# Performance work log

Hardware: AMD Instinct MI355X
Metric: run time of the kernel (lower is better)

The kernel has to match this reference:

```python
import jax, jax.numpy as jnp
import numpy as np

# config[4]: SparseConv3d(32, 64, k=3, stride=2, pad=1) on a (21,800,704) voxel grid, nnz=220939
IN_DIMS = (21, 800, 704)   # (x, y, z) spatial extents
KSIZE   = (3, 3, 3)
STRIDE  = (2, 2, 2)
PAD     = (1, 1, 1)
CIN, COUT = 32, 64
NNZ = 220939
OUT_DIMS = tuple((IN_DIMS[d] + 2 * PAD[d] - KSIZE[d]) // STRIDE[d] + 1 for d in range(3))  # (11,400,352)


def setup_inputs() -> dict:
    key = jax.random.key(0)
    k1, k2, k3 = jax.random.split(key, 3)
    features = jax.random.normal(k1, (NNZ, CIN), dtype=jnp.float32)
    coords = jnp.stack(
        [jax.random.randint(jax.random.fold_in(k2, d), (NNZ,), 0, IN_DIMS[d]) for d in range(3)],
        axis=1,
    ).astype(jnp.int32)
    # spconv weight layout: one [Cin, Cout] GEMM per kernel offset (27 offsets)
    weight = jax.random.normal(k3, (KSIZE[0] * KSIZE[1] * KSIZE[2], CIN, COUT), dtype=jnp.float32) * 0.05
    return {"features": features, "coords": coords, "weight": weight}


def reference(features, coords, weight):
    # Rulebook gather-GEMM-scatter, vectorized over points; static loop over 27 offsets.
    # out[o] += W[k] @ in[i] where i = o*stride - pad + k, i.e. o = (coord_i + pad - k)/stride.
    n_out = OUT_DIMS[0] * OUT_DIMS[1] * OUT_DIMS[2]
    stride = jnp.array(STRIDE, jnp.int32)
    pad = jnp.array(PAD, jnp.int32)
    odims = jnp.array(OUT_DIMS, jnp.int32)
    out = jnp.zeros((n_out + 1, COUT), features.dtype)  # last row = dump slot for invalid
    kidx = 0
    for kx in range(KSIZE[0]):
        for ky in range(KSIZE[1]):
            for kz in range(KSIZE[2]):
                off = jnp.array([kx, ky, kz], jnp.int32)
                o = coords + pad - off                      # [N,3]
                oq = o // stride
                valid = jnp.all((o >= 0) & (o % stride == 0) & (oq < odims), axis=1)
                flat = (oq[:, 0] * OUT_DIMS[1] + oq[:, 1]) * OUT_DIMS[2] + oq[:, 2]
                flat = jnp.where(valid, flat, n_out)
                contrib = features @ weight[kidx]           # [N, Cout] per-offset GEMM
                out = out.at[flat].add(contrib)             # scatter-accumulate
                kidx += 1
    # Densified sparse-conv output (inactive output sites are exactly zero)
    return out[:-1].reshape(OUT_DIMS + (COUT,))
```

## Files before the change

kernel.cpp:

```cpp
#include <hip/hip_runtime.h>


#define CIN    32
#define COUT   64
#define OXD    11
#define OYD    400
#define OZD    352
#define NOUT   (OXD * OYD * OZD)
#define BSITES 128
#define NBUCK  (NOUT / BSITES)
#define CAP    256
#define OVCAP  32768
#define NWT    (27 * COUT * CIN)

typedef float v2f __attribute__((ext_vector_type(2)));

__global__ __launch_bounds__(256) void prep(const float* __restrict__ w,
                                            float* __restrict__ wt,
                                            int* __restrict__ gcnt,
                                            int* __restrict__ ovcnt) {
    const int i = blockIdx.x * 256 + threadIdx.x;
    if (i < NWT) {
        const int k  = i >> 11;
        const int rm = i & 2047;
        const int co = rm >> 5;
        const int ci = rm & 31;
        wt[i] = w[k * (CIN * COUT) + ci * COUT + co];
    }
    if (i < NBUCK) gcnt[i] = 0;
    if (i == NBUCK) *ovcnt = 0;
}

__global__ __launch_bounds__(256) void build_pairs(
    const int* __restrict__ coords,
    int* __restrict__ arena,
    int* __restrict__ gcnt,
    int* __restrict__ ovcnt,
    int2* __restrict__ ovlist,
    int nnz)
{
    const int n = blockIdx.x * 256 + threadIdx.x;
    if (n >= nnz) return;

    const int cx = coords[3 * n + 0];
    const int cy = coords[3 * n + 1];
    const int cz = coords[3 * n + 2];

    int kxl[2], oxl[2], nx;
    int kyl[2], oyl[2], ny;
    int kzl[2], ozl[2], nz;
    {
        const int c1 = cx + 1;
        if (c1 & 1) { kxl[0] = 1; oxl[0] = c1 >> 1; nx = 1; }
        else { kxl[0] = 2; oxl[0] = (c1 - 2) >> 1; nx = 1;
               if ((c1 >> 1) < OXD) { kxl[1] = 0; oxl[1] = c1 >> 1; nx = 2; } }
    }
    {
        const int c1 = cy + 1;
        if (c1 & 1) { kyl[0] = 1; oyl[0] = c1 >> 1; ny = 1; }
        else { kyl[0] = 2; oyl[0] = (c1 - 2) >> 1; ny = 1;
               if ((c1 >> 1) < OYD) { kyl[1] = 0; oyl[1] = c1 >> 1; ny = 2; } }
    }
    {
        const int c1 = cz + 1;
        if (c1 & 1) { kzl[0] = 1; ozl[0] = c1 >> 1; nz = 1; }
        else { kzl[0] = 2; ozl[0] = (c1 - 2) >> 1; nz = 1;
               if ((c1 >> 1) < OZD) { kzl[1] = 0; ozl[1] = c1 >> 1; nz = 2; } }
    }

    for (int ix = 0; ix < nx; ++ix)
        for (int iy = 0; iy < ny; ++iy)
            for (int iz = 0; iz < nz; ++iz) {
                const int k    = kxl[ix] * 9 + kyl[iy] * 3 + kzl[iz];
                const int site = (oxl[ix] * OYD + oyl[iy]) * OZD + ozl[iz];
                const int bkt  = site >> 7;
                const int loc  = site & (BSITES - 1);
                const int slot = atomicAdd(&gcnt[bkt], 1);
                if (slot < CAP) {
                    arena[(size_t)bkt * CAP + slot] = (n << 12) | (k << 7) | loc;
                } else {
                    const int o = atomicAdd(ovcnt, 1);
                    if (o < OVCAP) ovlist[o] = make_int2(site, (n << 5) | k);
                }
            }
}

__global__ __launch_bounds__(256, 4) void spconv_scatter(
    const float* __restrict__ feat,
    const float* __restrict__ wt,
    const int*   __restrict__ arena,
    const int*   __restrict__ gcnt,
    float*       __restrict__ out)
{
    __shared__ float tile[BSITES][COUT];
    __shared__ int   sorted[CAP];
    __shared__ int   khist[27];
    __shared__ int   kbase[27];

    const int t    = threadIdx.x;
    const int lane = t & 63;
    const int wid  = t >> 6;
    const int b    = blockIdx.x;
    const int cnt  = min(gcnt[b], CAP);

    if (t < 27) khist[t] = 0;
    __syncthreads();

    int myp = 0, myk = 0;
    if (t < cnt) {
        myp = arena[(size_t)b * CAP + t];
        myk = (myp >> 7) & 31;
        atomicAdd(&khist[myk], 1);
    }
    float4* t4 = (float4*)&tile[0][0];
    #pragma unroll
    for (int r = 0; r < 8; ++r) t4[t + r * 256] = make_float4(0.f, 0.f, 0.f, 0.f);
    __syncthreads();

    if (wid == 0) {
        const int h = (lane < 27) ? khist[lane] : 0;
        int v = h;
        #pragma unroll
        for (int off = 1; off < 32; off <<= 1) {
            const int u = __shfl_up(v, off);
            if (lane >= off) v += u;
        }
        if (lane < 27) kbase[lane] = v - h;
    }
    __syncthreads();
    if (t < cnt) {
        const int pos = atomicAdd(&kbase[myk], 1);
        sorted[pos] = myp;
    }
    __syncthreads();

    const int c  = (cnt + 3) >> 2;
    const int jb = min(wid * c, cnt);
    const int je = min(jb + c, cnt);
    float4 wv[8];
    int curk = -1;
    for (int j = jb; j < je; ++j) {
        const int pk  = __builtin_amdgcn_readfirstlane(sorted[j]);
        const int k   = (pk >> 7) & 31;
        const int loc = pk & (BSITES - 1);
        const int pt  = pk >> 12;
        if (k != curk) {
            curk = k;
            const float4* __restrict__ wp =
                (const float4*)(wt + ((size_t)k * COUT + lane) * CIN);
            #pragma unroll
            for (int bb = 0; bb < 8; ++bb) wv[bb] = wp[bb];
        }
        const float4* __restrict__ fp = (const float4*)(feat + (size_t)pt * CIN);
        v2f a0 = {0.f, 0.f}, a1 = {0.f, 0.f};
        #pragma unroll
        for (int bb = 0; bb < 8; ++bb) {
            const float4 f = fp[bb];
            const float4 wb = wv[bb];
            v2f f01 = {f.x, f.y}, f23 = {f.z, f.w};
            v2f w01 = {wb.x, wb.y}, w23 = {wb.z, wb.w};
#if __has_builtin(__builtin_elementwise_fma)
            a0 = __builtin_elementwise_fma(f01, w01, a0);
            a1 = __builtin_elementwise_fma(f23, w23, a1);
#else
            a0[0] = fmaf(f01[0], w01[0], a0[0]);
            a0[1] = fmaf(f01[1], w01[1], a0[1]);
            a1[0] = fmaf(f23[0], w23[0], a1[0]);
            a1[1] = fmaf(f23[1], w23[1], a1[1]);
#endif
        }
        atomicAdd(&tile[loc][lane], (a0[0] + a0[1]) + (a1[0] + a1[1]));
    }
    __syncthreads();

    float4* __restrict__ o4 = (float4*)(out + (size_t)b * (BSITES * COUT));
    #pragma unroll
    for (int r = 0; r < 8; ++r) o4[t + r * 256] = t4[t + r * 256];
}

__global__ __launch_bounds__(256) void fixup_overflow(
    const float* __restrict__ feat,
    const float* __restrict__ wt,
    const int2*  __restrict__ ovlist,
    const int*   __restrict__ ovcnt,
    float*       __restrict__ out)
{
    const int lane = threadIdx.x & 63;
    const int gw   = blockIdx.x * 4 + (threadIdx.x >> 6);
    const int n    = min(*ovcnt, OVCAP);
    for (int e = gw; e < n; e += 128 * 4) {
        const int2 r   = ovlist[e];
        const int site = r.x;
        const int pt   = r.y >> 5;
        const int k    = r.y & 31;
        const float4* __restrict__ wp =
            (const float4*)(wt + ((size_t)k * COUT + lane) * CIN);
        const float4* __restrict__ fp = (const float4*)(feat + (size_t)pt * CIN);
        float acc = 0.f;
        #pragma unroll
        for (int bb = 0; bb < 8; ++bb) {
            const float4 f = fp[bb];
            const float4 w = wp[bb];
            acc = fmaf(f.x, w.x, acc);
            acc = fmaf(f.y, w.y, acc);
            acc = fmaf(f.z, w.z, acc);
            acc = fmaf(f.w, w.w, acc);
        }
        atomicAdd(out + (size_t)site * COUT + lane, acc);
    }
}

extern "C" void kernel_launch(void* const* d_in, const int* in_sizes, int n_in,
                              void* d_out, int out_size, void* d_ws, size_t ws_size,
                              hipStream_t stream) {
    const float* feat   = (const float*)d_in[0];
    const int*   coords = (const int*)d_in[1];
    const float* weight = (const float*)d_in[2];
    float*       out    = (float*)d_out;
    const int nnz = in_sizes[0] / CIN;

    float* WT     = (float*)d_ws;
    int*   gcnt   = (int*)(WT + NWT);
    int*   ovcnt  = gcnt + NBUCK;
    int2*  ovlist = (int2*)(ovcnt + 2);
    int*   arena  = (int*)(ovlist + OVCAP);

    prep<<<(NWT + 255) / 256, 256, 0, stream>>>(weight, WT, gcnt, ovcnt);
    build_pairs<<<(nnz + 255) / 256, 256, 0, stream>>>(coords, arena, gcnt,
                                                       ovcnt, ovlist, nnz);
    spconv_scatter<<<NBUCK, 256, 0, stream>>>(feat, WT, arena, gcnt, out);
    fixup_overflow<<<128, 256, 0, stream>>>(feat, WT, ovlist, ovcnt, out);
}
```

Before: 675.8 us.

## Stage feature rows cooperatively in LDS and pad bucket counters

Each wave now loads the pair list into registers once. It then fetches feature rows 16 at a time with coalesced per-lane float4 loads into a swizzled LDS staging buffer. Before, every lane re-read the same row from global memory for each pair in sequence. This exposes more memory-level parallelism and cuts redundant broadcast loads. Bucket counters are spread 16 ints apart so atomics on neighbouring buckets do not share a cache line, and spconv_scatter's launch-bounds occupancy hint drops from 4 to 3 blocks to leave room for the extra LDS and registers.

Result: slower. 715.8 us (+5.9%).

```diff
diff --git a/kernel.cpp b/kernel.cpp
--- a/kernel.cpp
+++ b/kernel.cpp
@@ -10,6 +10,7 @@
 #define BSITES 128
 #define NBUCK  (NOUT / BSITES)
 #define CAP    256
+#define GSTR   16
 #define OVCAP  32768
 #define NWT    (27 * COUT * CIN)
 
@@ -27,8 +28,8 @@
         const int ci = rm & 31;
         wt[i] = w[k * (CIN * COUT) + ci * COUT + co];
     }
-    if (i < NBUCK) gcnt[i] = 0;
-    if (i == NBUCK) *ovcnt = 0;
+    if (i < NBUCK) gcnt[i * GSTR] = 0;
+    if (i == 0) *ovcnt = 0;
 }
 
 __global__ __launch_bounds__(256) void build_pairs(
@@ -75,7 +76,7 @@
                 const int site = (oxl[ix] * OYD + oyl[iy]) * OZD + ozl[iz];
                 const int bkt  = site >> 7;
                 const int loc  = site & (BSITES - 1);
-                const int slot = atomicAdd(&gcnt[bkt], 1);
+                const int slot = atomicAdd(&gcnt[bkt * GSTR], 1);
                 if (slot < CAP) {
                     arena[(size_t)bkt * CAP + slot] = (n << 12) | (k << 7) | loc;
                 } else {
@@ -85,7 +86,7 @@
             }
 }
 
-__global__ __launch_bounds__(256, 4) void spconv_scatter(
+__global__ __launch_bounds__(256, 3) void spconv_scatter(
     const float* __restrict__ feat,
     const float* __restrict__ wt,
     const int*   __restrict__ arena,
@@ -93,6 +94,7 @@
     float*       __restrict__ out)
 {
     __shared__ float tile[BSITES][COUT];
+    __shared__ float fstage[4][16 * 32];
     __shared__ int   sorted[CAP];
     __shared__ int   khist[27];
     __shared__ int   kbase[27];
@@ -101,7 +103,7 @@
     const int lane = t & 63;
     const int wid  = t >> 6;
     const int b    = blockIdx.x;
-    const int cnt  = min(gcnt[b], CAP);
+    const int cnt  = min(gcnt[b * GSTR], CAP);
 
     if (t < 27) khist[t] = 0;
     __syncthreads();
@@ -137,39 +139,60 @@
     const int c  = (cnt + 3) >> 2;
     const int jb = min(wid * c, cnt);
     const int je = min(jb + c, cnt);
+
+    const int vp = sorted[(jb + lane < je) ? (jb + lane) : (je > jb ? je - 1 : 0)];
+
+    float* __restrict__ fs = &fstage[wid][0];
     float4 wv[8];
     int curk = -1;
-    for (int j = jb; j < je; ++j) {
-        const int pk  = __builtin_amdgcn_readfirstlane(sorted[j]);
-        const int k   = (pk >> 7) & 31;
-        const int loc = pk & (BSITES - 1);
-        const int pt  = pk >> 12;
-        if (k != curk) {
-            curk = k;
-            const float4* __restrict__ wp =
-                (const float4*)(wt + ((size_t)k * COUT + lane) * CIN);
+
+    for (int g0 = jb; g0 < je; g0 += 16) {
+        #pragma unroll
+        for (int i = 0; i < 2; ++i) {
+            const int r   = (lane >> 3) + 8 * i;
+            const int s   = min(g0 - jb + r, je - 1 - jb);
+            const int pv  = __shfl(vp, s);
+            const int pt  = pv >> 12;
+            const int ch  = lane & 7;
+            const float4 v = ((const float4*)(feat + (size_t)pt * CIN))[ch];
+            const int sw  = ch ^ (r & 7);
+            *(float4*)(fs + (r * 8 + sw) * 4) = v;
+        }
+        asm volatile("s_waitcnt lgkmcnt(0)" ::: "memory");
+
+        const int jend = min(g0 + 16, je);
+        for (int j = g0; j < jend; ++j) {
+            const int pk  = __builtin_amdgcn_readlane(vp, j - jb);
+            const int k   = (pk >> 7) & 31;
+            const int loc = pk & (BSITES - 1);
+            const int r   = j - g0;
+            if (k != curk) {
+                curk = k;
+                const float4* __restrict__ wp =
+                    (const float4*)(wt + ((size_t)k * COUT + lane) * CIN);
+                #pragma unroll
+                for (int bb = 0; bb < 8; ++bb) wv[bb] = wp[bb];
+            }
+            v2f a0 = {0.f, 0.f}, a1 = {0.f, 0.f};
             #pragma unroll
-            for (int bb = 0; bb < 8; ++bb) wv[bb] = wp[bb];
-        }
-        const float4* __restrict__ fp = (const float4*)(feat + (size_t)pt * CIN);
-        v2f a0 = {0.f, 0.f}, a1 = {0.f, 0.f};
-        #pragma unroll
-        for (int bb = 0; bb < 8; ++bb) {
-            const float4 f = fp[bb];
-            const float4 wb = wv[bb];
-            v2f f01 = {f.x, f.y}, f23 = {f.z, f.w};
-            v2f w01 = {wb.x, wb.y}, w23 = {wb.z, wb.w};
+            for (int bb = 0; bb < 8; ++bb) {
+                const float4 f =
+                    *(const float4*)(fs + (r * 8 + (bb ^ (r & 7))) * 4);
+                const float4 wb = wv[bb];
+                v2f f01 = {f.x, f.y}, f23 = {f.z, f.w};
+                v2f w01 = {wb.x, wb.y}, w23 = {wb.z, wb.w};
 #if __has_builtin(__builtin_elementwise_fma)
-            a0 = __builtin_elementwise_fma(f01, w01, a0);
-            a1 = __builtin_elementwise_fma(f23, w23, a1);
+                a0 = __builtin_elementwise_fma(f01, w01, a0);
+                a1 = __builtin_elementwise_fma(f23, w23, a1);
 #else
-            a0[0] = fmaf(f01[0], w01[0], a0[0]);
-            a0[1] = fmaf(f01[1], w01[1], a0[1]);
-            a1[0] = fmaf(f23[0], w23[0], a1[0]);
-            a1[1] = fmaf(f23[1], w23[1], a1[1]);
+                a0[0] = fmaf(f01[0], w01[0], a0[0]);
+                a0[1] = fmaf(f01[1], w01[1], a0[1]);
+                a1[0] = fmaf(f23[0], w23[0], a1[0]);
+                a1[1] = fmaf(f23[1], w23[1], a1[1]);
 #endif
-        }
-        atomicAdd(&tile[loc][lane], (a0[0] + a0[1]) + (a1[0] + a1[1]));
+            }
+            atomicAdd(&tile[loc][lane], (a0[0] + a0[1]) + (a1[0] + a1[1]));
+        }
     }
     __syncthreads();
 
@@ -221,7 +244,7 @@
 
     float* WT     = (float*)d_ws;
     int*   gcnt   = (int*)(WT + NWT);
-    int*   ovcnt  = gcnt + NBUCK;
+    int*   ovcnt  = gcnt + NBUCK * GSTR;
     int2*  ovlist = (int2*)(ovcnt + 2);
     int*   arena  = (int*)(ovlist + OVCAP);
 
```

## Replace bucketed scatter rulebook with dense voxel map and per-output gather

Applied to the files above, without the earlier changes.

Swaps the atomic-bucketed pair arena for a dense input-voxel index map filled by atomicExch. Each output block then probes the 27 neighbours of its sites through the map and accumulates contributions in a shared-memory tile. Duplicate coordinates go to a dup list that a fixup kernel scatters with global atomics. This removes the global bucket atomics and the in-block sort, but adds clearing a ~47MB map and many mostly-empty random probes.

Measured after the change: 929.8 us. +37.6%, slower.

```diff
diff --git a/kernel.cpp b/kernel.cpp
--- a/kernel.cpp
+++ b/kernel.cpp
@@ -3,23 +3,28 @@
 
 #define CIN    32
 #define COUT   64
+#define IXD    21
+#define IYD    800
+#define IZD    704
 #define OXD    11
 #define OYD    400
 #define OZD    352
 #define NOUT   (OXD * OYD * OZD)
+#define NVOX   (IXD * IYD * IZD)
+#define NVOX4  (NVOX / 4)
 #define BSITES 128
-#define NBUCK  (NOUT / BSITES)
-#define CAP    256
-#define OVCAP  32768
+#define NBLK   (NOUT / BSITES)
 #define NWT    (27 * COUT * CIN)
+#define DUPCAP 48000
 
 typedef float v2f __attribute__((ext_vector_type(2)));
 
 __global__ __launch_bounds__(256) void prep(const float* __restrict__ w,
+                                            int4* __restrict__ map4,
                                             float* __restrict__ wt,
-                                            int* __restrict__ gcnt,
-                                            int* __restrict__ ovcnt) {
+                                            int* __restrict__ dupcnt) {
     const int i = blockIdx.x * 256 + threadIdx.x;
+    if (i < NVOX4) map4[i] = make_int4(-1, -1, -1, -1);
     if (i < NWT) {
         const int k  = i >> 11;
         const int rm = i & 2047;
@@ -27,186 +32,182 @@
         const int ci = rm & 31;
         wt[i] = w[k * (CIN * COUT) + ci * COUT + co];
     }
-    if (i < NBUCK) gcnt[i] = 0;
-    if (i == NBUCK) *ovcnt = 0;
-}
-
-__global__ __launch_bounds__(256) void build_pairs(
+    if (i == 0) *dupcnt = 0;
+}
+
+__global__ __launch_bounds__(256) void build_map(
     const int* __restrict__ coords,
-    int* __restrict__ arena,
-    int* __restrict__ gcnt,
-    int* __restrict__ ovcnt,
-    int2* __restrict__ ovlist,
+    int* __restrict__ map,
+    int* __restrict__ dupcnt,
+    int* __restrict__ duplist,
     int nnz)
 {
     const int n = blockIdx.x * 256 + threadIdx.x;
     if (n >= nnz) return;
-
     const int cx = coords[3 * n + 0];
     const int cy = coords[3 * n + 1];
     const int cz = coords[3 * n + 2];
-
-    int kxl[2], oxl[2], nx;
-    int kyl[2], oyl[2], ny;
-    int kzl[2], ozl[2], nz;
-    {
-        const int c1 = cx + 1;
-        if (c1 & 1) { kxl[0] = 1; oxl[0] = c1 >> 1; nx = 1; }
-        else { kxl[0] = 2; oxl[0] = (c1 - 2) >> 1; nx = 1;
-               if ((c1 >> 1) < OXD) { kxl[1] = 0; oxl[1] = c1 >> 1; nx = 2; } }
-    }
-    {
-        const int c1 = cy + 1;
-        if (c1 & 1) { kyl[0] = 1; oyl[0] = c1 >> 1; ny = 1; }
-        else { kyl[0] = 2; oyl[0] = (c1 - 2) >> 1; ny = 1;
-               if ((c1 >> 1) < OYD) { kyl[1] = 0; oyl[1] = c1 >> 1; ny = 2; } }
-    }
-    {
-        const int c1 = cz + 1;
-        if (c1 & 1) { kzl[0] = 1; ozl[0] = c1 >> 1; nz = 1; }
-        else { kzl[0] = 2; ozl[0] = (c1 - 2) >> 1; nz = 1;
-               if ((c1 >> 1) < OZD) { kzl[1] = 0; ozl[1] = c1 >> 1; nz = 2; } }
-    }
-
-    for (int ix = 0; ix < nx; ++ix)
-        for (int iy = 0; iy < ny; ++iy)
-            for (int iz = 0; iz < nz; ++iz) {
-                const int k    = kxl[ix] * 9 + kyl[iy] * 3 + kzl[iz];
-                const int site = (oxl[ix] * OYD + oyl[iy]) * OZD + ozl[iz];
-                const int bkt  = site >> 7;
-                const int loc  = site & (BSITES - 1);
-                const int slot = atomicAdd(&gcnt[bkt], 1);
-                if (slot < CAP) {
-                    arena[(size_t)bkt * CAP + slot] = (n << 12) | (k << 7) | loc;
-                } else {
-                    const int o = atomicAdd(ovcnt, 1);
-                    if (o < OVCAP) ovlist[o] = make_int2(site, (n << 5) | k);
-                }
-            }
-}
-
-__global__ __launch_bounds__(256, 4) void spconv_scatter(
+    const int v  = (cx * IYD + cy) * IZD + cz;
+    const int old = atomicExch(&map[v], n);
+    if (old >= 0) {
+        const int s = atomicAdd(dupcnt, 1);
+        if (s < DUPCAP) duplist[s] = old;
+    }
+}
+
+__global__ __launch_bounds__(256, 4) void spconv_gather(
     const float* __restrict__ feat,
     const float* __restrict__ wt,
-    const int*   __restrict__ arena,
-    const int*   __restrict__ gcnt,
+    const int*   __restrict__ map,
     float*       __restrict__ out)
 {
     __shared__ float tile[BSITES][COUT];
-    __shared__ int   sorted[CAP];
-    __shared__ int   khist[27];
-    __shared__ int   kbase[27];
 
     const int t    = threadIdx.x;
     const int lane = t & 63;
     const int wid  = t >> 6;
-    const int b    = blockIdx.x;
-    const int cnt  = min(gcnt[b], CAP);
-
-    if (t < 27) khist[t] = 0;
-    __syncthreads();
-
-    int myp = 0, myk = 0;
-    if (t < cnt) {
-        myp = arena[(size_t)b * CAP + t];
-        myk = (myp >> 7) & 31;
-        atomicAdd(&khist[myk], 1);
-    }
+
     float4* t4 = (float4*)&tile[0][0];
     #pragma unroll
     for (int r = 0; r < 8; ++r) t4[t + r * 256] = make_float4(0.f, 0.f, 0.f, 0.f);
     __syncthreads();
 
-    if (wid == 0) {
-        const int h = (lane < 27) ? khist[lane] : 0;
-        int v = h;
+    const int ls   = lane & 31;
+    const int site = blockIdx.x * BSITES + wid * 32 + ls;
+    const int ox   = site / (OYD * OZD);
+    const int r0   = site - ox * (OYD * OZD);
+    const int oy   = r0 / OZD;
+    const int oz   = r0 - oy * OZD;
+    const int ix0  = 2 * ox - 1;
+    const int iy0  = 2 * oy - 1;
+    const int iz0  = 2 * oz - 1;
+    const int kh   = lane >> 5;
+
+    auto probe = [&](int kp) -> int {
+        const int kk = kp + kh;
+        if (kk >= 27) return -1;
+        const int kx = kk / 9;
+        const int kr = kk - kx * 9;
+        const int ky = kr / 3;
+        const int kz = kr - ky * 3;
+        const int ix = ix0 + kx, iy = iy0 + ky, iz = iz0 + kz;
+        if ((unsigned)ix >= IXD || (unsigned)iy >= IYD || (unsigned)iz >= IZD)
+            return -1;
+        return map[(ix * IYD + iy) * IZD + iz];
+    };
+
+    int v = probe(0);
+    for (int kp = 0; kp < 27; kp += 2) {
+        const int vnext = (kp + 2 < 27) ? probe(kp + 2) : -1;
+        const unsigned long long bal = __ballot(v >= 0);
         #pragma unroll
-        for (int off = 1; off < 32; off <<= 1) {
-            const int u = __shfl_up(v, off);
-            if (lane >= off) v += u;
-        }
-        if (lane < 27) kbase[lane] = v - h;
-    }
-    __syncthreads();
-    if (t < cnt) {
-        const int pos = atomicAdd(&kbase[myk], 1);
-        sorted[pos] = myp;
-    }
-    __syncthreads();
-
-    const int c  = (cnt + 3) >> 2;
-    const int jb = min(wid * c, cnt);
-    const int je = min(jb + c, cnt);
-    float4 wv[8];
-    int curk = -1;
-    for (int j = jb; j < je; ++j) {
-        const int pk  = __builtin_amdgcn_readfirstlane(sorted[j]);
-        const int k   = (pk >> 7) & 31;
-        const int loc = pk & (BSITES - 1);
-        const int pt  = pk >> 12;
-        if (k != curk) {
-            curk = k;
+        for (int s = 0; s < 2; ++s) {
+            const int k = kp + s;
+            if (k >= 27) break;
+            unsigned mask = (unsigned)(bal >> (32 * s));
+            if (mask == 0) continue;
+            float4 wv[8];
             const float4* __restrict__ wp =
                 (const float4*)(wt + ((size_t)k * COUT + lane) * CIN);
             #pragma unroll
-            for (int bb = 0; bb < 8; ++bb) wv[bb] = wp[bb];
-        }
-        const float4* __restrict__ fp = (const float4*)(feat + (size_t)pt * CIN);
-        v2f a0 = {0.f, 0.f}, a1 = {0.f, 0.f};
-        #pragma unroll
-        for (int bb = 0; bb < 8; ++bb) {
-            const float4 f = fp[bb];
-            const float4 wb = wv[bb];
-            v2f f01 = {f.x, f.y}, f23 = {f.z, f.w};
-            v2f w01 = {wb.x, wb.y}, w23 = {wb.z, wb.w};
+            for (int b = 0; b < 8; ++b) wv[b] = wp[b];
+            do {
+                const int bit = __builtin_ctz(mask);
+                mask &= mask - 1;
+                const int p = __builtin_amdgcn_readlane(v, 32 * s + bit);
+                const float4* __restrict__ fr4 =
+                    (const float4*)(feat + (size_t)p * CIN);
+                float4 fr[8];
+                #pragma unroll
+                for (int b = 0; b < 8; ++b) fr[b] = fr4[b];
+                v2f a0 = {0.f, 0.f}, a1 = {0.f, 0.f};
+                #pragma unroll
+                for (int b = 0; b < 8; ++b) {
+                    v2f f01 = {fr[b].x, fr[b].y}, f23 = {fr[b].z, fr[b].w};
+                    v2f w01 = {wv[b].x, wv[b].y}, w23 = {wv[b].z, wv[b].w};
 #if __has_builtin(__builtin_elementwise_fma)
-            a0 = __builtin_elementwise_fma(f01, w01, a0);
-            a1 = __builtin_elementwise_fma(f23, w23, a1);
+                    a0 = __builtin_elementwise_fma(f01, w01, a0);
+                    a1 = __builtin_elementwise_fma(f23, w23, a1);
 #else
-            a0[0] = fmaf(f01[0], w01[0], a0[0]);
-            a0[1] = fmaf(f01[1], w01[1], a0[1]);
-            a1[0] = fmaf(f23[0], w23[0], a1[0]);
-            a1[1] = fmaf(f23[1], w23[1], a1[1]);
+                    a0[0] = fmaf(f01[0], w01[0], a0[0]);
+                    a0[1] = fmaf(f01[1], w01[1], a0[1]);
+                    a1[0] = fmaf(f23[0], w23[0], a1[0]);
+                    a1[1] = fmaf(f23[1], w23[1], a1[1]);
 #endif
-        }
-        atomicAdd(&tile[loc][lane], (a0[0] + a0[1]) + (a1[0] + a1[1]));
+                }
+                atomicAdd(&tile[wid * 32 + bit][lane],
+                          (a0[0] + a0[1]) + (a1[0] + a1[1]));
+            } while (mask);
+        }
+        v = vnext;
     }
     __syncthreads();
 
-    float4* __restrict__ o4 = (float4*)(out + (size_t)b * (BSITES * COUT));
+    float4* __restrict__ o4 = (float4*)(out + (size_t)blockIdx.x * (BSITES * COUT));
     #pragma unroll
     for (int r = 0; r < 8; ++r) o4[t + r * 256] = t4[t + r * 256];
 }
 
-__global__ __launch_bounds__(256) void fixup_overflow(
+__global__ __launch_bounds__(256) void fixup_dups(
     const float* __restrict__ feat,
     const float* __restrict__ wt,
-    const int2*  __restrict__ ovlist,
-    const int*   __restrict__ ovcnt,
+    const int*   __restrict__ coords,
+    const int*   __restrict__ duplist,
+    const int*   __restrict__ dupcnt,
     float*       __restrict__ out)
 {
     const int lane = threadIdx.x & 63;
     const int gw   = blockIdx.x * 4 + (threadIdx.x >> 6);
-    const int n    = min(*ovcnt, OVCAP);
-    for (int e = gw; e < n; e += 128 * 4) {
-        const int2 r   = ovlist[e];
-        const int site = r.x;
-        const int pt   = r.y >> 5;
-        const int k    = r.y & 31;
-        const float4* __restrict__ wp =
-            (const float4*)(wt + ((size_t)k * COUT + lane) * CIN);
-        const float4* __restrict__ fp = (const float4*)(feat + (size_t)pt * CIN);
-        float acc = 0.f;
+    const int n    = min(*dupcnt, DUPCAP);
+    for (int e = gw; e < n; e += 64 * 4) {
+        const int p  = duplist[e];
+        const int cx = coords[3 * p + 0];
+        const int cy = coords[3 * p + 1];
+        const int cz = coords[3 * p + 2];
+        int kxl[2], oxl[2], nx;
+        int kyl[2], oyl[2], ny;
+        int kzl[2], ozl[2], nz;
+        {
+            const int c1 = cx + 1;
+            if (c1 & 1) { kxl[0] = 1; oxl[0] = c1 >> 1; nx = 1; }
+            else { kxl[0] = 2; oxl[0] = (c1 - 2) >> 1; nx = 1;
+                   if ((c1 >> 1) < OXD) { kxl[1] = 0; oxl[1] = c1 >> 1; nx = 2; } }
+        }
+        {
+            const int c1 = cy + 1;
+            if (c1 & 1) { kyl[0] = 1; oyl[0] = c1 >> 1; ny = 1; }
+            else { kyl[0] = 2; oyl[0] = (c1 - 2) >> 1; ny = 1;
+                   if ((c1 >> 1) < OYD) { kyl[1] = 0; oyl[1] = c1 >> 1; ny = 2; } }
+        }
+        {
+            const int c1 = cz + 1;
+            if (c1 & 1) { kzl[0] = 1; ozl[0] = c1 >> 1; nz = 1; }
+            else { kzl[0] = 2; ozl[0] = (c1 - 2) >> 1; nz = 1;
+                   if ((c1 >> 1) < OZD) { kzl[1] = 0; ozl[1] = c1 >> 1; nz = 2; } }
+        }
+        const float4* __restrict__ fp = (const float4*)(feat + (size_t)p * CIN);
+        float4 fr[8];
         #pragma unroll
-        for (int bb = 0; bb < 8; ++bb) {
-            const float4 f = fp[bb];
-            const float4 w = wp[bb];
-            acc = fmaf(f.x, w.x, acc);
-            acc = fmaf(f.y, w.y, acc);
-            acc = fmaf(f.z, w.z, acc);
-            acc = fmaf(f.w, w.w, acc);
-        }
-        atomicAdd(out + (size_t)site * COUT + lane, acc);
+        for (int b = 0; b < 8; ++b) fr[b] = fp[b];
+        for (int ix = 0; ix < nx; ++ix)
+            for (int iy = 0; iy < ny; ++iy)
+                for (int iz = 0; iz < nz; ++iz) {
+                    const int k    = kxl[ix] * 9 + kyl[iy] * 3 + kzl[iz];
+                    const int site = (oxl[ix] * OYD + oyl[iy]) * OZD + ozl[iz];
+                    const float4* __restrict__ wp =
+                        (const float4*)(wt + ((size_t)k * COUT + lane) * CIN);
+                    float acc = 0.f;
+                    #pragma unroll
+                    for (int b = 0; b < 8; ++b) {
+                        const float4 f = fr[b];
+                        const float4 w = wp[b];
+                        acc = fmaf(f.x, w.x, acc);
+                        acc = fmaf(f.y, w.y, acc);
+                        acc = fmaf(f.z, w.z, acc);
+                        acc = fmaf(f.w, w.w, acc);
+                    }
+                    atomicAdd(out + (size_t)site * COUT + lane, acc);
+                }
     }
 }
 
@@ -219,15 +220,14 @@
     float*       out    = (float*)d_out;
     const int nnz = in_sizes[0] / CIN;
 
-    float* WT     = (float*)d_ws;
-    int*   gcnt   = (int*)(WT + NWT);
-    int*   ovcnt  = gcnt + NBUCK;
-    int2*  ovlist = (int2*)(ovcnt + 2);
-    int*   arena  = (int*)(ovlist + OVCAP);
-
-    prep<<<(NWT + 255) / 256, 256, 0, stream>>>(weight, WT, gcnt, ovcnt);
-    build_pairs<<<(nnz + 255) / 256, 256, 0, stream>>>(coords, arena, gcnt,
-                                                       ovcnt, ovlist, nnz);
-    spconv_scatter<<<NBUCK, 256, 0, stream>>>(feat, WT, arena, gcnt, out);
-    fixup_overflow<<<128, 256, 0, stream>>>(feat, WT, ovlist, ovcnt, out);
-}
+    int*   map     = (int*)d_ws;
+    float* WT      = (float*)(map + NVOX);
+    int*   dupcnt  = (int*)(WT + NWT);
+    int*   duplist = dupcnt + 4;
+
+    prep<<<(NVOX4 + 255) / 256, 256, 0, stream>>>(weight, (int4*)map, WT, dupcnt);
+    build_map<<<(nnz + 255) / 256, 256, 0, stream>>>(coords, map, dupcnt,
+                                                     duplist, nnz);
+    spconv_gather<<<NBLK, 256, 0, stream>>>(feat, WT, map, out);
+    fixup_dups<<<64, 256, 0, stream>>>(feat, WT, coords, duplist, dupcnt, out);
+}
```

## Split sparse conv into per-offset GEMM and bucketed reduction with fp16 partials

Applied to the files above, without the earlier changes.

Pair building now emits two rulebooks: one grouped by kernel offset, filled through per-block shared-memory histograms and a single global atomic per offset, and one grouped by output bucket whose entries index into per-offset partial-product rows. A new per-offset kernel computes the 32x64 product for every pair and stores fp16 partials. The reduce kernel then only gathers those rows and accumulates them into a shared tile, so the per-bucket sorting and weight reloads go away. This adds a large intermediate buffer plus an extra pass, fp16 rounding of the partials, and a heavier overflow path when the per-offset capacity derived from workspace size is exceeded.

New measurement: 801.5 us. 18.6% more time.

```diff
diff --git a/kernel.cpp b/kernel.cpp
--- a/kernel.cpp
+++ b/kernel.cpp
@@ -10,14 +10,20 @@
 #define BSITES 128
 #define NBUCK  (NOUT / BSITES)
 #define CAP    256
-#define OVCAP  32768
+#define GSTR   16
 #define NWT    (27 * COUT * CIN)
+#define CHA    32
+#define PCAPK_MAX 32768
+#define OVCAP  600000
 
 typedef float v2f __attribute__((ext_vector_type(2)));
+typedef _Float16 half_t;
+typedef _Float16 h8 __attribute__((ext_vector_type(8)));
 
 __global__ __launch_bounds__(256) void prep(const float* __restrict__ w,
                                             float* __restrict__ wt,
-                                            int* __restrict__ gcnt,
+                                            int* __restrict__ kcnt,
+                                            int* __restrict__ bcnt,
                                             int* __restrict__ ovcnt) {
     const int i = blockIdx.x * 256 + threadIdx.x;
     if (i < NWT) {
@@ -27,149 +33,189 @@
         const int ci = rm & 31;
         wt[i] = w[k * (CIN * COUT) + ci * COUT + co];
     }
-    if (i < NBUCK) gcnt[i] = 0;
-    if (i == NBUCK) *ovcnt = 0;
-}
-
-__global__ __launch_bounds__(256) void build_pairs(
+    if (i < NBUCK) bcnt[i * GSTR] = 0;
+    if (i < 32)    kcnt[i] = 0;
+    if (i == 0)    *ovcnt = 0;
+}
+
+__global__ __launch_bounds__(512) void build_pairs(
     const int* __restrict__ coords,
-    int* __restrict__ arena,
-    int* __restrict__ gcnt,
+    int* __restrict__ arenaA,
+    int* __restrict__ arenaB,
+    int* __restrict__ kcnt,
+    int* __restrict__ bcnt,
     int* __restrict__ ovcnt,
     int2* __restrict__ ovlist,
-    int nnz)
-{
-    const int n = blockIdx.x * 256 + threadIdx.x;
-    if (n >= nnz) return;
-
-    const int cx = coords[3 * n + 0];
-    const int cy = coords[3 * n + 1];
-    const int cz = coords[3 * n + 2];
-
-    int kxl[2], oxl[2], nx;
-    int kyl[2], oyl[2], ny;
-    int kzl[2], ozl[2], nz;
-    {
-        const int c1 = cx + 1;
-        if (c1 & 1) { kxl[0] = 1; oxl[0] = c1 >> 1; nx = 1; }
-        else { kxl[0] = 2; oxl[0] = (c1 - 2) >> 1; nx = 1;
-               if ((c1 >> 1) < OXD) { kxl[1] = 0; oxl[1] = c1 >> 1; nx = 2; } }
-    }
-    {
-        const int c1 = cy + 1;
-        if (c1 & 1) { kyl[0] = 1; oyl[0] = c1 >> 1; ny = 1; }
-        else { kyl[0] = 2; oyl[0] = (c1 - 2) >> 1; ny = 1;
-               if ((c1 >> 1) < OYD) { kyl[1] = 0; oyl[1] = c1 >> 1; ny = 2; } }
-    }
-    {
-        const int c1 = cz + 1;
-        if (c1 & 1) { kzl[0] = 1; ozl[0] = c1 >> 1; nz = 1; }
-        else { kzl[0] = 2; ozl[0] = (c1 - 2) >> 1; nz = 1;
-               if ((c1 >> 1) < OZD) { kzl[1] = 0; ozl[1] = c1 >> 1; nz = 2; } }
-    }
-
-    for (int ix = 0; ix < nx; ++ix)
-        for (int iy = 0; iy < ny; ++iy)
-            for (int iz = 0; iz < nz; ++iz) {
-                const int k    = kxl[ix] * 9 + kyl[iy] * 3 + kzl[iz];
-                const int site = (oxl[ix] * OYD + oyl[iy]) * OZD + ozl[iz];
-                const int bkt  = site >> 7;
-                const int loc  = site & (BSITES - 1);
-                const int slot = atomicAdd(&gcnt[bkt], 1);
-                if (slot < CAP) {
-                    arena[(size_t)bkt * CAP + slot] = (n << 12) | (k << 7) | loc;
-                } else {
-                    const int o = atomicAdd(ovcnt, 1);
-                    if (o < OVCAP) ovlist[o] = make_int2(site, (n << 5) | k);
+    int nnz, int pcapk)
+{
+    __shared__ int lcnt[27];
+    __shared__ int lbase[27];
+    const int t = threadIdx.x;
+    if (t < 27) lcnt[t] = 0;
+    __syncthreads();
+
+    const int n = blockIdx.x * 512 + t;
+    int ncomb = 0;
+    int ck[8], cls[8], csite[8];
+    if (n < nnz) {
+        const int cx = coords[3 * n + 0];
+        const int cy = coords[3 * n + 1];
+        const int cz = coords[3 * n + 2];
+        int kxl[2], oxl[2], nx;
+        int kyl[2], oyl[2], ny;
+        int kzl[2], ozl[2], nz;
+        {
+            const int c1 = cx + 1;
+            if (c1 & 1) { kxl[0] = 1; oxl[0] = c1 >> 1; nx = 1; }
+            else { kxl[0] = 2; oxl[0] = (c1 - 2) >> 1; nx = 1;
+                   if ((c1 >> 1) < OXD) { kxl[1] = 0; oxl[1] = c1 >> 1; nx = 2; } }
+        }
+        {
+            const int c1 = cy + 1;
+            if (c1 & 1) { kyl[0] = 1; oyl[0] = c1 >> 1; ny = 1; }
+            else { kyl[0] = 2; oyl[0] = (c1 - 2) >> 1; ny = 1;
+                   if ((c1 >> 1) < OYD) { kyl[1] = 0; oyl[1] = c1 >> 1; ny = 2; } }
+        }
+        {
+            const int c1 = cz + 1;
+            if (c1 & 1) { kzl[0] = 1; ozl[0] = c1 >> 1; nz = 1; }
+            else { kzl[0] = 2; ozl[0] = (c1 - 2) >> 1; nz = 1;
+                   if ((c1 >> 1) < OZD) { kzl[1] = 0; ozl[1] = c1 >> 1; nz = 2; } }
+        }
+        for (int ix = 0; ix < nx; ++ix)
+            for (int iy = 0; iy < ny; ++iy)
+                for (int iz = 0; iz < nz; ++iz) {
+                    const int k = kxl[ix] * 9 + kyl[iy] * 3 + kzl[iz];
+                    ck[ncomb]    = k;
+                    csite[ncomb] = (oxl[ix] * OYD + oyl[iy]) * OZD + ozl[iz];
+                    cls[ncomb]   = atomicAdd(&lcnt[k], 1);
+                    ++ncomb;
                 }
+    }
+    __syncthreads();
+    if (t < 27) lbase[t] = atomicAdd(&kcnt[t], lcnt[t]);
+    __syncthreads();
+
+    for (int c = 0; c < ncomb; ++c) {
+        const int k     = ck[c];
+        const int site  = csite[c];
+        const int slotk = lbase[k] + cls[c];
+        if (slotk < pcapk) {
+            arenaA[(size_t)k * pcapk + slotk] = n;
+            const int bkt = site >> 7;
+            const int loc = site & (BSITES - 1);
+            const int sb  = atomicAdd(&bcnt[bkt * GSTR], 1);
+            if (sb < CAP) {
+                arenaB[(size_t)bkt * CAP + sb] = ((k * pcapk + slotk) << 7) | loc;
+            } else {
+                const int o = atomicAdd(ovcnt, 1);
+                if (o < OVCAP) ovlist[o] = make_int2(site, (n << 5) | k);
             }
-}
-
-__global__ __launch_bounds__(256, 4) void spconv_scatter(
+        } else {
+            const int o = atomicAdd(ovcnt, 1);
+            if (o < OVCAP) ovlist[o] = make_int2(site, (n << 5) | k);
+        }
+    }
+}
+
+__global__ __launch_bounds__(256, 3) void gemm_k(
     const float* __restrict__ feat,
     const float* __restrict__ wt,
-    const int*   __restrict__ arena,
-    const int*   __restrict__ gcnt,
-    float*       __restrict__ out)
+    const int*   __restrict__ arenaA,
+    const int*   __restrict__ kcnt,
+    half_t*      __restrict__ P16,
+    int pcapk)
+{
+    const int lane = threadIdx.x & 63;
+    const int wid  = threadIdx.x >> 6;
+    const int k     = blockIdx.x % 27;
+    const int chunk = blockIdx.x / 27;
+    const int cnt = min(kcnt[k], pcapk);
+    if (cnt == 0) return;
+
+    const int NW    = CHA * 4;
+    const int widk  = chunk * 4 + wid;
+    const int C     = (cnt + NW - 1) / NW;
+    const int start = min(widk * C, cnt);
+    const int end   = min(start + C, cnt);
+    const float* __restrict__ Wk = wt + (size_t)k * (COUT * CIN);
+    const int*   __restrict__ ak = arenaA + (size_t)k * pcapk;
+    half_t*      __restrict__ Pk = P16 + (size_t)k * pcapk * COUT;
+
+    for (int i0 = start; i0 < end; i0 += 64) {
+        const int idx = i0 + lane;
+        const int pt  = ak[min(idx, end - 1)];
+
+        v2f f[16];
+        {
+            const float4* __restrict__ fr4 = (const float4*)(feat + (size_t)pt * CIN);
+            #pragma unroll
+            for (int b = 0; b < 8; ++b) {
+                const float4 v = fr4[b];
+                f[2 * b + 0] = (v2f){v.x, v.y};
+                f[2 * b + 1] = (v2f){v.z, v.w};
+            }
+        }
+
+        if (idx < end) {
+            half_t* __restrict__ prow = Pk + (size_t)idx * COUT;
+            #pragma unroll
+            for (int g = 0; g < 8; ++g) {
+                h8 res;
+                #pragma unroll
+                for (int u = 0; u < 8; ++u) {
+                    const int co = 8 * g + u;
+                    const v2f* __restrict__ wv = (const v2f*)(Wk + co * CIN);
+                    v2f a = {0.f, 0.f};
+                    #pragma unroll
+                    for (int c2 = 0; c2 < 16; ++c2) {
+#if __has_builtin(__builtin_elementwise_fma)
+                        a = __builtin_elementwise_fma(f[c2], wv[c2], a);
+#else
+                        a[0] = fmaf(f[c2][0], wv[c2][0], a[0]);
+                        a[1] = fmaf(f[c2][1], wv[c2][1], a[1]);
+#endif
+                    }
+                    res[u] = (half_t)(a[0] + a[1]);
+                }
+                *(h8*)(prow + 8 * g) = res;
+            }
+        }
+    }
+}
+
+__global__ __launch_bounds__(256, 4) void reduce_b(
+    const half_t* __restrict__ P16,
+    const int*    __restrict__ arenaB,
+    const int*    __restrict__ bcnt,
+    float*        __restrict__ out)
 {
     __shared__ float tile[BSITES][COUT];
-    __shared__ int   sorted[CAP];
-    __shared__ int   khist[27];
-    __shared__ int   kbase[27];
 
     const int t    = threadIdx.x;
     const int lane = t & 63;
     const int wid  = t >> 6;
     const int b    = blockIdx.x;
-    const int cnt  = min(gcnt[b], CAP);
-
-    if (t < 27) khist[t] = 0;
-    __syncthreads();
-
-    int myp = 0, myk = 0;
-    if (t < cnt) {
-        myp = arena[(size_t)b * CAP + t];
-        myk = (myp >> 7) & 31;
-        atomicAdd(&khist[myk], 1);
-    }
+    const int cnt  = min(bcnt[b * GSTR], CAP);
+
     float4* t4 = (float4*)&tile[0][0];
     #pragma unroll
     for (int r = 0; r < 8; ++r) t4[t + r * 256] = make_float4(0.f, 0.f, 0.f, 0.f);
     __syncthreads();
 
-    if (wid == 0) {
-        const int h = (lane < 27) ? khist[lane] : 0;
-        int v = h;
-        #pragma unroll
-        for (int off = 1; off < 32; off <<= 1) {
-            const int u = __shfl_up(v, off);
-            if (lane >= off) v += u;
-        }
-        if (lane < 27) kbase[lane] = v - h;
-    }
-    __syncthreads();
-    if (t < cnt) {
-        const int pos = atomicAdd(&kbase[myk], 1);
-        sorted[pos] = myp;
-    }
-    __syncthreads();
-
     const int c  = (cnt + 3) >> 2;
     const int jb = min(wid * c, cnt);
     const int je = min(jb + c, cnt);
-    float4 wv[8];
-    int curk = -1;
+    const int* __restrict__ ab = arenaB + (size_t)b * CAP;
+    const int myw = ab[(jb + lane < je) ? (jb + lane) : (je > jb ? je - 1 : 0)];
+
+    #pragma unroll 8
     for (int j = jb; j < je; ++j) {
-        const int pk  = __builtin_amdgcn_readfirstlane(sorted[j]);
-        const int k   = (pk >> 7) & 31;
-        const int loc = pk & (BSITES - 1);
-        const int pt  = pk >> 12;
-        if (k != curk) {
-            curk = k;
-            const float4* __restrict__ wp =
-                (const float4*)(wt + ((size_t)k * COUT + lane) * CIN);
-            #pragma unroll
-            for (int bb = 0; bb < 8; ++bb) wv[bb] = wp[bb];
-        }
-        const float4* __restrict__ fp = (const float4*)(feat + (size_t)pt * CIN);
-        v2f a0 = {0.f, 0.f}, a1 = {0.f, 0.f};
-        #pragma unroll
-        for (int bb = 0; bb < 8; ++bb) {
-            const float4 f = fp[bb];
-            const float4 wb = wv[bb];
-            v2f f01 = {f.x, f.y}, f23 = {f.z, f.w};
-            v2f w01 = {wb.x, wb.y}, w23 = {wb.z, wb.w};
-#if __has_builtin(__builtin_elementwise_fma)
-            a0 = __builtin_elementwise_fma(f01, w01, a0);
-            a1 = __builtin_elementwise_fma(f23, w23, a1);
-#else
-            a0[0] = fmaf(f01[0], w01[0], a0[0]);
-            a0[1] = fmaf(f01[1], w01[1], a0[1]);
-            a1[0] = fmaf(f23[0], w23[0], a1[0]);
-            a1[1] = fmaf(f23[1], w23[1], a1[1]);
-#endif
-        }
-        atomicAdd(&tile[loc][lane], (a0[0] + a0[1]) + (a1[0] + a1[1]));
+        const int w    = __builtin_amdgcn_readlane(myw, j - jb);
+        const int prow = w >> 7;
+        const int loc  = w & (BSITES - 1);
+        const float h  = (float)P16[(size_t)prow * COUT + lane];
+        atomicAdd(&tile[loc][lane], h);
     }
     __syncthreads();
 
@@ -188,19 +234,19 @@
     const int lane = threadIdx.x & 63;
     const int gw   = blockIdx.x * 4 + (threadIdx.x >> 6);
     const int n    = min(*ovcnt, OVCAP);
-    for (int e = gw; e < n; e += 128 * 4) {
+    for (int e = gw; e < n; e += 64 * 4) {
         const int2 r   = ovlist[e];
         const int site = r.x;
-        const int pt   = r.y >> 5;
+        const int p    = r.y >> 5;
         const int k    = r.y & 31;
         const float4* __restrict__ wp =
             (const float4*)(wt + ((size_t)k * COUT + lane) * CIN);
-        const float4* __restrict__ fp = (const float4*)(feat + (size_t)pt * CIN);
+        const float4* __restrict__ fp = (const float4*)(feat + (size_t)p * CIN);
         float acc = 0.f;
         #pragma unroll
-        for (int bb = 0; bb < 8; ++bb) {
-            const float4 f = fp[bb];
-            const float4 w = wp[bb];
+        for (int b = 0; b < 8; ++b) {
+            const float4 f = fp[b];
+            const float4 w = wp[b];
             acc = fmaf(f.x, w.x, acc);
             acc = fmaf(f.y, w.y, acc);
             acc = fmaf(f.z, w.z, acc);
@@ -220,14 +266,27 @@
     const int nnz = in_sizes[0] / CIN;
 
     float* WT     = (float*)d_ws;
-    int*   gcnt   = (int*)(WT + NWT);
-    int*   ovcnt  = gcnt + NBUCK;
-    int2*  ovlist = (int2*)(ovcnt + 2);
-    int*   arena  = (int*)(ovlist + OVCAP);
-
-    prep<<<(NWT + 255) / 256, 256, 0, stream>>>(weight, WT, gcnt, ovcnt);
-    build_pairs<<<(nnz + 255) / 256, 256, 0, stream>>>(coords, arena, gcnt,
-                                                       ovcnt, ovlist, nnz);
-    spconv_scatter<<<NBUCK, 256, 0, stream>>>(feat, WT, arena, gcnt, out);
-    fixup_overflow<<<128, 256, 0, stream>>>(feat, WT, ovlist, ovcnt, out);
-}
+    int*   kcnt   = (int*)(WT + NWT);
+    int*   bcnt   = kcnt + 32;
+    int*   ovcnt  = bcnt + NBUCK * GSTR;
+    int*   arenaB = ovcnt + 4;
+    int2*  ovlist = (int2*)(arenaB + (size_t)NBUCK * CAP);
+    int*   arenaA = (int*)(ovlist + OVCAP);
+    const size_t fixed = (size_t)((char*)arenaA - (char*)d_ws);
+
+    long avail = (long)ws_size - (long)fixed - 512;
+    int pcapk = (int)(avail / (27L * (sizeof(int) + COUT * sizeof(half_t))));
+    if (pcapk > PCAPK_MAX) pcapk = PCAPK_MAX;
+    if (pcapk < 1024)      pcapk = 1024;
+    uintptr_t pa = (uintptr_t)(arenaA + (size_t)27 * pcapk);
+    pa = (pa + 255) & ~(uintptr_t)255;
+    half_t* P16 = (half_t*)pa;
+
+    prep<<<(NWT + 255) / 256, 256, 0, stream>>>(weight, WT, kcnt, bcnt, ovcnt);
+    build_pairs<<<(nnz + 511) / 512, 512, 0, stream>>>(coords, arenaA, arenaB,
+                                                       kcnt, bcnt, ovcnt,
+                                                       ovlist, nnz, pcapk);
+    gemm_k<<<27 * CHA, 256, 0, stream>>>(feat, WT, arenaA, kcnt, P16, pcapk);
+    reduce_b<<<NBUCK, 256, 0, stream>>>(P16, arenaB, bcnt, out);
+    fixup_overflow<<<64, 256, 0, stream>>>(feat, WT, ovlist, ovcnt, out);
+}
```
